# Performance work log

Measured on AMD Instinct MI355X. Metric: run time of the kernel, lower is better.

The kernel has to match this reference:

```python
import jax, jax.numpy as jnp
import numpy as np


def setup_inputs() -> dict:
    key = jax.random.key(0)
    k1, k2 = jax.random.split(key)
    inputs = jax.random.normal(k1, (16, 64, 64, 64), dtype=jnp.float32)  # NCHW, C=embedding_dim
    codebook = jax.random.normal(k2, (1024, 64), dtype=jnp.float32)      # [K, D]
    return {"inputs": inputs, "codebook": codebook}


def reference(inputs, codebook):
    # inputs: [B, C, H, W] -> [B, H, W, C] -> [N, D]
    D = codebook.shape[1]
    x = jnp.transpose(inputs, (0, 2, 3, 1)).reshape(-1, D)  # [N, D]
    distances = (
        jnp.sum(x * x, axis=1, keepdims=True)
        + jnp.sum(codebook * codebook, axis=1)
        - 2.0 * jnp.matmul(x, codebook.T)
    )
    encoding_indices = jnp.argmin(distances, axis=1)[:, None]  # [N, 1]
    return encoding_indices
```

## Files before the change

kernel.cpp:

```cpp
#include <hip/hip_runtime.h>


typedef float f4 __attribute__((ext_vector_type(4)));
typedef short s8v __attribute__((ext_vector_type(8)));
typedef unsigned int u32;

#define D_DIM 64
#define HW    4096
#define ROWS  64
#define INF_  __builtin_inff()
#define MFMA(a,b,c) __builtin_amdgcn_mfma_f32_16x16x32_bf16(a,b,c,0,0,0)

__device__ __forceinline__ unsigned short bf_rne(float f) {
    u32 u = __builtin_bit_cast(u32, f);
    u32 r = u + 0x7fffu + ((u >> 16) & 1u);
    return (unsigned short)(r >> 16);
}
__device__ __forceinline__ float bf_to_f(unsigned short h) {
    u32 u = ((u32)h) << 16;
    return __builtin_bit_cast(float, u);
}
__device__ __forceinline__ void split3(float f, unsigned short& h,
                                       unsigned short& m, unsigned short& l) {
    h = bf_rne(f);
    float f1 = f - bf_to_f(h);
    m = bf_rne(f1);
    float f2 = f1 - bf_to_f(m);
    l = bf_rne(f2);
}
__device__ __forceinline__ s8v pack8(unsigned short a0, unsigned short a1,
                                     unsigned short a2, unsigned short a3,
                                     unsigned short a4, unsigned short a5,
                                     unsigned short a6, unsigned short a7) {
    uint4 u;
    u.x = a0 | ((u32)a1 << 16);
    u.y = a2 | ((u32)a3 << 16);
    u.z = a4 | ((u32)a5 << 16);
    u.w = a6 | ((u32)a7 << 16);
    return __builtin_bit_cast(s8v, u);
}

__global__ __launch_bounds__(64) void prep_kernel(const float* __restrict__ cb,
                                                  char* __restrict__ wsb) {
    const int blk = blockIdx.x;
    const int lane = threadIdx.x;
    if (blk < 384) {
        const int T = blk / 6;
        const int rem = blk - T * 6;
        const int s = rem / 3;
        const int L = rem - s * 3;
        const int code = T * 16 + (lane & 15);
        const int ch0 = s * 32 + (lane >> 4) * 8;
        const float* src = cb + code * 64 + ch0;
        unsigned short o[8];
#pragma unroll
        for (int j = 0; j < 8; ++j) {
            unsigned short h, m2, l;
            split3(src[j], h, m2, l);
            o[j] = (L == 0) ? h : (L == 1) ? m2 : l;
        }
        uint4 w;
        w.x = o[0] | ((u32)o[1] << 16);
        w.y = o[2] | ((u32)o[3] << 16);
        w.z = o[4] | ((u32)o[5] << 16);
        w.w = o[6] | ((u32)o[7] << 16);
        *(uint4*)(wsb + (size_t)blk * 1024 + lane * 16) = w;
    } else {
        const int k = (blk - 384) * 64 + lane;
        const f4* row = (const f4*)(cb + (size_t)k * 64);
        float sacc = 0.f;
#pragma unroll
        for (int i = 0; i < 16; ++i) {
            f4 v = row[i];
            sacc = fmaf(v.x, v.x, sacc);
            sacc = fmaf(v.y, v.y, sacc);
            sacc = fmaf(v.z, v.z, sacc);
            sacc = fmaf(v.w, v.w, sacc);
        }
        ((float*)(wsb + 384 * 1024))[k] = sacc;
    }
}

__device__ __forceinline__ void gl_lds16(const char* g, char* l) {
    __builtin_amdgcn_global_load_lds(
        (const __attribute__((address_space(1))) void*)g,
        (__attribute__((address_space(3))) void*)l, 16, 0, 0);
}

#define BUILD_A(s) { \
    const float* xr = (const float*)&xs4[w16 + m_][0]; \
    f4 va = *(const f4*)(xr + (s) * 32 + ko); \
    f4 vb = *(const f4*)(xr + (s) * 32 + ko + 4); \
    unsigned short h0,h1,h2,h3,h4,h5,h6,h7; \
    unsigned short q0,q1,q2,q3,q4,q5,q6,q7; \
    unsigned short l0,l1,l2,l3,l4,l5,l6,l7; \
    split3(-2.f * va.x, h0, q0, l0); split3(-2.f * va.y, h1, q1, l1); \
    split3(-2.f * va.z, h2, q2, l2); split3(-2.f * va.w, h3, q3, l3); \
    split3(-2.f * vb.x, h4, q4, l4); split3(-2.f * vb.y, h5, q5, l5); \
    split3(-2.f * vb.z, h6, q6, l6); split3(-2.f * vb.w, h7, q7, l7); \
    Ah##s = pack8(h0,h1,h2,h3,h4,h5,h6,h7); \
    Am##s = pack8(q0,q1,q2,q3,q4,q5,q6,q7); \
    Al##s = pack8(l0,l1,l2,l3,l4,l5,l6,l7); \
}

#define UPD1(t, i, en, kn) { \
    float v = a##t##a[i] + a##t##b[i] + (en); \
    bool pr = (v < best##i); \
    best##i = pr ? v : best##i; \
    idx##i  = pr ? (kn) : idx##i; \
}

#define Z4 (f4){0.f,0.f,0.f,0.f}

#define PHASE(CUR, P) { \
    const char* gsrc = wsb + (size_t)(((P) + 1) & 31) * 12288 + stageoff; \
    char* ldst = sB + (((CUR) ^ 1) * 12288) + w3072; \
    gl_lds16(gsrc,        ldst); \
    gl_lds16(gsrc + 1024, ldst + 1024); \
    gl_lds16(gsrc + 2048, ldst + 2048); \
    const char* bb = sB + (CUR) * 12288 + lane16; \
    s8v B0h0 = *(const s8v*)(bb +     0), B0m0 = *(const s8v*)(bb +  1024); \
    s8v B0l0 = *(const s8v*)(bb +  2048), B0h1 = *(const s8v*)(bb +  3072); \
    s8v B0m1 = *(const s8v*)(bb +  4096), B0l1 = *(const s8v*)(bb +  5120); \
    s8v B1h0 = *(const s8v*)(bb +  6144), B1m0 = *(const s8v*)(bb +  7168); \
    s8v B1l0 = *(const s8v*)(bb +  8192), B1h1 = *(const s8v*)(bb +  9216); \
    s8v B1m1 = *(const s8v*)(bb + 10240), B1l1 = *(const s8v*)(bb + 11264); \
    const float en0 = sEn[(P) * 32 + m_]; \
    const float en1 = sEn[(P) * 32 + 16 + m_]; \
    f4 a0a = Z4, a0b = Z4, a1a = Z4, a1b = Z4; \
    a0a = MFMA(Ah0,B0h0,a0a); a0b = MFMA(Ah1,B0h1,a0b); \
    a1a = MFMA(Ah0,B1h0,a1a); a1b = MFMA(Ah1,B1h1,a1b); \
    a0a = MFMA(Ah0,B0m0,a0a); a0b = MFMA(Ah1,B0m1,a0b); \
    a1a = MFMA(Ah0,B1m0,a1a); a1b = MFMA(Ah1,B1m1,a1b); \
    a0a = MFMA(Am0,B0h0,a0a); a0b = MFMA(Am1,B0h1,a0b); \
    a1a = MFMA(Am0,B1h0,a1a); a1b = MFMA(Am1,B1h1,a1b); \
    a0a = MFMA(Ah0,B0l0,a0a); a0b = MFMA(Ah1,B0l1,a0b); \
    a1a = MFMA(Ah0,B1l0,a1a); a1b = MFMA(Ah1,B1l1,a1b); \
    a0a = MFMA(Am0,B0m0,a0a); a0b = MFMA(Am1,B0m1,a0b); \
    a1a = MFMA(Am0,B1m0,a1a); a1b = MFMA(Am1,B1m1,a1b); \
    a0a = MFMA(Al0,B0h0,a0a); a0b = MFMA(Al1,B0h1,a0b); \
    a1a = MFMA(Al0,B1h0,a1a); a1b = MFMA(Al1,B1h1,a1b); \
    const int kn0 = (P) * 32 + m_; \
    UPD1(0,0,en0,kn0)    UPD1(0,1,en0,kn0)    UPD1(0,2,en0,kn0)    UPD1(0,3,en0,kn0) \
    UPD1(1,0,en1,kn0+16) UPD1(1,1,en1,kn0+16) UPD1(1,2,en1,kn0+16) UPD1(1,3,en1,kn0+16) \
    __syncthreads(); \
}

#define BF1(i, msk) { \
    float ov = __shfl_xor(best##i, msk); \
    int   oi = __shfl_xor(idx##i,  msk); \
    bool pr = (ov < best##i) || (ov == best##i && oi < idx##i); \
    best##i = pr ? ov : best##i; \
    idx##i  = pr ? oi : idx##i; \
}
#define BFALL(msk) BF1(0,msk) BF1(1,msk) BF1(2,msk) BF1(3,msk)

__global__ __launch_bounds__(256, 4) void vq_kernel(const float* __restrict__ x,
                                                    const char* __restrict__ wsb,
                                                    int* __restrict__ out) {
    __shared__ __align__(16) char smem[24576];
    __shared__ float sEn[1024];
    f4 (*xs4)[17] = (f4 (*)[17])smem;
    char* const sB = smem;

    const int tid = threadIdx.x;
    const int lane = tid & 63;
    const int w = __builtin_amdgcn_readfirstlane(tid >> 6);
    const int m_ = lane & 15;
    const int ko = (lane >> 4) * 8;
    const int w16 = w * 16;
    const int w3072 = w * 3072;
    const int lane16 = lane * 16;
    const int stageoff = w3072 + lane16;
    const int n0 = blockIdx.x * ROWS;
    const int b = n0 >> 12;
    const int hw0 = n0 & (HW - 1);

    const float* enp = (const float*)(wsb + 384 * 1024);
#pragma unroll
    for (int q = 0; q < 4; ++q) sEn[q * 256 + tid] = enp[q * 256 + tid];

    {
        const float* g = x + ((size_t)b * D_DIM + w16) * HW + hw0 + lane;
        float v[16];
#pragma unroll
        for (int i = 0; i < 16; ++i) v[i] = g[(size_t)i * HW];
#pragma unroll
        for (int j = 0; j < 4; ++j)
            xs4[lane][w * 4 + j] = (f4){v[4*j], v[4*j+1], v[4*j+2], v[4*j+3]};
    }
    __syncthreads();

    s8v Ah0, Am0, Al0, Ah1, Am1, Al1;
    BUILD_A(0) BUILD_A(1)
    __syncthreads();

    {
        const char* g0 = wsb + stageoff;
        char* l0 = sB + w3072;
        gl_lds16(g0,        l0);
        gl_lds16(g0 + 1024, l0 + 1024);
        gl_lds16(g0 + 2048, l0 + 2048);
    }

    float best0 = INF_, best1 = INF_, best2 = INF_, best3 = INF_;
    int idx0 = 0, idx1 = 0, idx2 = 0, idx3 = 0;
    __syncthreads();

#pragma unroll 1
    for (int pp = 0; pp < 16; ++pp) {
        PHASE(0, pp * 2)
        PHASE(1, pp * 2 + 1)
    }

    BFALL(1) BFALL(2) BFALL(4) BFALL(8)

    if (m_ == 0) {
        int4 o4; o4.x = idx0; o4.y = idx1; o4.z = idx2; o4.w = idx3;
        *(int4*)(out + n0 + w16 + (lane >> 4) * 4) = o4;
    }
}

extern "C" void kernel_launch(void* const* d_in, const int* in_sizes, int n_in,
                              void* d_out, int out_size, void* d_ws, size_t ws_size,
                              hipStream_t stream) {
    const float* x  = (const float*)d_in[0];
    const float* cb = (const float*)d_in[1];
    char* wsb = (char*)d_ws;
    int*  out = (int*)d_out;

    prep_kernel<<<dim3(400), dim3(64), 0, stream>>>(cb, wsb);
    vq_kernel<<<dim3(65536 / ROWS), dim3(256), 0, stream>>>(x, wsb, out);
}
```

Measured before the change: 108.6 us.

## Triple-buffer codebook staging with partial vmcnt waits and MFMA priority

Replaces the double-buffered LDS staging of codebook tiles with a three-buffer ring, prefetching two phases ahead. The per-phase __syncthreads is replaced by an explicit s_waitcnt vmcnt(3) plus s_barrier, so only the oldest outstanding global-to-LDS load must finish before the barrier. s_setprio is raised around the MFMA block. LDS use grows from 24KB to 36KB per block, which may reduce occupancy below the 4 blocks per CU declared in launch_bounds.

```diff
diff --git a/kernel.cpp b/kernel.cpp
--- a/kernel.cpp
+++ b/kernel.cpp
@@ -112,40 +112,6 @@
 
 #define Z4 (f4){0.f,0.f,0.f,0.f}
 
-#define PHASE(CUR, P) { \
-    const char* gsrc = wsb + (size_t)(((P) + 1) & 31) * 12288 + stageoff; \
-    char* ldst = sB + (((CUR) ^ 1) * 12288) + w3072; \
-    gl_lds16(gsrc,        ldst); \
-    gl_lds16(gsrc + 1024, ldst + 1024); \
-    gl_lds16(gsrc + 2048, ldst + 2048); \
-    const char* bb = sB + (CUR) * 12288 + lane16; \
-    s8v B0h0 = *(const s8v*)(bb +     0), B0m0 = *(const s8v*)(bb +  1024); \
-    s8v B0l0 = *(const s8v*)(bb +  2048), B0h1 = *(const s8v*)(bb +  3072); \
-    s8v B0m1 = *(const s8v*)(bb +  4096), B0l1 = *(const s8v*)(bb +  5120); \
-    s8v B1h0 = *(const s8v*)(bb +  6144), B1m0 = *(const s8v*)(bb +  7168); \
-    s8v B1l0 = *(const s8v*)(bb +  8192), B1h1 = *(const s8v*)(bb +  9216); \
-    s8v B1m1 = *(const s8v*)(bb + 10240), B1l1 = *(const s8v*)(bb + 11264); \
-    const float en0 = sEn[(P) * 32 + m_]; \
-    const float en1 = sEn[(P) * 32 + 16 + m_]; \
-    f4 a0a = Z4, a0b = Z4, a1a = Z4, a1b = Z4; \
-    a0a = MFMA(Ah0,B0h0,a0a); a0b = MFMA(Ah1,B0h1,a0b); \
-    a1a = MFMA(Ah0,B1h0,a1a); a1b = MFMA(Ah1,B1h1,a1b); \
-    a0a = MFMA(Ah0,B0m0,a0a); a0b = MFMA(Ah1,B0m1,a0b); \
-    a1a = MFMA(Ah0,B1m0,a1a); a1b = MFMA(Ah1,B1m1,a1b); \
-    a0a = MFMA(Am0,B0h0,a0a); a0b = MFMA(Am1,B0h1,a0b); \
-    a1a = MFMA(Am0,B1h0,a1a); a1b = MFMA(Am1,B1h1,a1b); \
-    a0a = MFMA(Ah0,B0l0,a0a); a0b = MFMA(Ah1,B0l1,a0b); \
-    a1a = MFMA(Ah0,B1l0,a1a); a1b = MFMA(Ah1,B1l1,a1b); \
-    a0a = MFMA(Am0,B0m0,a0a); a0b = MFMA(Am1,B0m1,a0b); \
-    a1a = MFMA(Am0,B1m0,a1a); a1b = MFMA(Am1,B1m1,a1b); \
-    a0a = MFMA(Al0,B0h0,a0a); a0b = MFMA(Al1,B0h1,a0b); \
-    a1a = MFMA(Al0,B1h0,a1a); a1b = MFMA(Al1,B1h1,a1b); \
-    const int kn0 = (P) * 32 + m_; \
-    UPD1(0,0,en0,kn0)    UPD1(0,1,en0,kn0)    UPD1(0,2,en0,kn0)    UPD1(0,3,en0,kn0) \
-    UPD1(1,0,en1,kn0+16) UPD1(1,1,en1,kn0+16) UPD1(1,2,en1,kn0+16) UPD1(1,3,en1,kn0+16) \
-    __syncthreads(); \
-}
-
 #define BF1(i, msk) { \
     float ov = __shfl_xor(best##i, msk); \
     int   oi = __shfl_xor(idx##i,  msk); \
@@ -158,7 +124,7 @@
 __global__ __launch_bounds__(256, 4) void vq_kernel(const float* __restrict__ x,
                                                     const char* __restrict__ wsb,
                                                     int* __restrict__ out) {
-    __shared__ __align__(16) char smem[24576];
+    __shared__ __align__(16) char smem[36864];
     __shared__ float sEn[1024];
     f4 (*xs4)[17] = (f4 (*)[17])smem;
     char* const sB = smem;
@@ -169,9 +135,9 @@
     const int m_ = lane & 15;
     const int ko = (lane >> 4) * 8;
     const int w16 = w * 16;
-    const int w3072 = w * 3072;
+    const int wu = w * 3072;
     const int lane16 = lane * 16;
-    const int stageoff = w3072 + lane16;
+    const int stageoff = wu + lane16;
     const int n0 = blockIdx.x * ROWS;
     const int b = n0 >> 12;
     const int hw0 = n0 & (HW - 1);
@@ -195,23 +161,72 @@
     BUILD_A(0) BUILD_A(1)
     __syncthreads();
 
-    {
-        const char* g0 = wsb + stageoff;
-        char* l0 = sB + w3072;
-        gl_lds16(g0,        l0);
-        gl_lds16(g0 + 1024, l0 + 1024);
-        gl_lds16(g0 + 2048, l0 + 2048);
-    }
+    char* b0 = sB;
+    char* b1 = sB + 12288;
+    char* b2 = sB + 24576;
+
+    gl_lds16(wsb + stageoff,                b0 + wu);
+    gl_lds16(wsb + stageoff + 1024,         b0 + wu + 1024);
+    gl_lds16(wsb + stageoff + 2048,         b0 + wu + 2048);
+    gl_lds16(wsb + 12288 + stageoff,        b1 + wu);
+    gl_lds16(wsb + 12288 + stageoff + 1024, b1 + wu + 1024);
+    gl_lds16(wsb + 12288 + stageoff + 2048, b1 + wu + 2048);
 
     float best0 = INF_, best1 = INF_, best2 = INF_, best3 = INF_;
     int idx0 = 0, idx1 = 0, idx2 = 0, idx3 = 0;
-    __syncthreads();
+
+    asm volatile("s_waitcnt vmcnt(3)" ::: "memory");
+    __builtin_amdgcn_s_barrier();
+
+    const char* gp = wsb + 2 * 12288;
+    const char* const gend = wsb + 32 * 12288;
+    int p32 = 0;
 
 #pragma unroll 1
-    for (int pp = 0; pp < 16; ++pp) {
-        PHASE(0, pp * 2)
-        PHASE(1, pp * 2 + 1)
-    }
+    for (int pp = 0; pp < 32; ++pp) {
+        gl_lds16(gp + stageoff,        b2 + wu);
+        gl_lds16(gp + stageoff + 1024, b2 + wu + 1024);
+        gl_lds16(gp + stageoff + 2048, b2 + wu + 2048);
+
+        const char* bb = b0 + lane16;
+        s8v B0h0 = *(const s8v*)(bb +     0), B0m0 = *(const s8v*)(bb +  1024);
+        s8v B0l0 = *(const s8v*)(bb +  2048), B0h1 = *(const s8v*)(bb +  3072);
+        s8v B0m1 = *(const s8v*)(bb +  4096), B0l1 = *(const s8v*)(bb +  5120);
+        s8v B1h0 = *(const s8v*)(bb +  6144), B1m0 = *(const s8v*)(bb +  7168);
+        s8v B1l0 = *(const s8v*)(bb +  8192), B1h1 = *(const s8v*)(bb +  9216);
+        s8v B1m1 = *(const s8v*)(bb + 10240), B1l1 = *(const s8v*)(bb + 11264);
+        const float en0 = sEn[p32 + m_];
+        const float en1 = sEn[p32 + 16 + m_];
+
+        f4 a0a = Z4, a0b = Z4, a1a = Z4, a1b = Z4;
+        __builtin_amdgcn_s_setprio(1);
+        a0a = MFMA(Ah0,B0h0,a0a); a0b = MFMA(Ah1,B0h1,a0b);
+        a1a = MFMA(Ah0,B1h0,a1a); a1b = MFMA(Ah1,B1h1,a1b);
+        a0a = MFMA(Ah0,B0m0,a0a); a0b = MFMA(Ah1,B0m1,a0b);
+        a1a = MFMA(Ah0,B1m0,a1a); a1b = MFMA(Ah1,B1m1,a1b);
+        a0a = MFMA(Am0,B0h0,a0a); a0b = MFMA(Am1,B0h1,a0b);
+        a1a = MFMA(Am0,B1h0,a1a); a1b = MFMA(Am1,B1h1,a1b);
+        a0a = MFMA(Ah0,B0l0,a0a); a0b = MFMA(Ah1,B0l1,a0b);
+        a1a = MFMA(Ah0,B1l0,a1a); a1b = MFMA(Ah1,B1l1,a1b);
+        a0a = MFMA(Am0,B0m0,a0a); a0b = MFMA(Am1,B0m1,a0b);
+        a1a = MFMA(Am0,B1m0,a1a); a1b = MFMA(Am1,B1m1,a1b);
+        a0a = MFMA(Al0,B0h0,a0a); a0b = MFMA(Al1,B0h1,a0b);
+        a1a = MFMA(Al0,B1h0,a1a); a1b = MFMA(Al1,B1h1,a1b);
+        __builtin_amdgcn_s_setprio(0);
+
+        const int kn0 = p32 + m_;
+        UPD1(0,0,en0,kn0)    UPD1(0,1,en0,kn0)    UPD1(0,2,en0,kn0)    UPD1(0,3,en0,kn0)
+        UPD1(1,0,en1,kn0+16) UPD1(1,1,en1,kn0+16) UPD1(1,2,en1,kn0+16) UPD1(1,3,en1,kn0+16)
+
+        asm volatile("s_waitcnt vmcnt(3) lgkmcnt(0)" ::: "memory");
+        __builtin_amdgcn_s_barrier();
+
+        { char* t = b0; b0 = b1; b1 = b2; b2 = t; }
+        gp += 12288;
+        if (gp == gend) gp = wsb;
+        p32 += 32;
+    }
+    asm volatile("s_waitcnt vmcnt(0)" ::: "memory");
 
     BFALL(1) BFALL(2) BFALL(4) BFALL(8)
 
```

Result: no change. 109.7 us (+1.0%).
